# Kernel optimization log

Hardware: AMD Instinct MI355X
Metric: run time of the kernel (lower is better)

The kernel has to match this reference:

```python
import jax, jax.numpy as jnp
import numpy as np
import math

W = 64  # window_size == chunk_size == 64


def _windows(x, w):
    """x: [b, t, ...] -> [b, nb, 2w, ...]: for block j, concat(block j-1, block j).
    Block -1 is zero padding; its validity is handled by the attention mask."""
    b, t = x.shape[0], x.shape[1]
    nb = t // w
    pad = [(0, 0), (w, 0)] + [(0, 0)] * (x.ndim - 2)
    xp = jnp.pad(x, pad)                                   # [b, t+w, ...]
    xb = xp.reshape((b, nb + 1, w) + x.shape[2:])          # [b, nb+1, w, ...]
    return jnp.concatenate([xb[:, :-1], xb[:, 1:]], axis=2)  # [b, nb, 2w, ...]


def setup_inputs() -> dict:
    key = jax.random.key(0)
    k1, k2, k3 = jax.random.split(key, 3)
    b, t, h, d = 4, 4096, 16, 64
    return {
        "q": jax.random.normal(k1, (b, t, h, d), dtype=jnp.float32),
        "k": jax.random.normal(k2, (b, t, h, d), dtype=jnp.float32),
        "v": jax.random.normal(k3, (b, t, h, d), dtype=jnp.float32),
        "attn_mask": jnp.ones((b, t), dtype=jnp.int32),
    }


def reference(q, k, v, attn_mask):
    b, t, h, d = q.shape
    nb = t // W
    scale = 1.0 / math.sqrt(d)

    qb = q.reshape(b, nb, W, h, d)
    kw = _windows(k, W)                         # [b, nb, 2W, h, d]
    vw = _windows(v, W)                         # [b, nb, 2W, h, d]
    mw = _windows(attn_mask.astype(bool), W)    # [b, nb, 2W]

    # query local index i attends to key local index m iff 0 <= (i+W-m) < W
    i = jnp.arange(W)[:, None]
    m = jnp.arange(2 * W)[None, :]
    diff = i + W - m
    band = (diff >= 0) & (diff < W)             # [W, 2W]

    valid = band[None, None] & mw[:, :, None, :]          # [b, nb, W, 2W]

    scores = jnp.einsum('bnqhd,bnkhd->bnhqk', qb, kw) * scale  # [b,nb,h,W,2W]
    scores = jnp.where(valid[:, :, None], scores, jnp.float32(-1e9))
    attn = jax.nn.softmax(scores, axis=-1)
    attn = attn * valid[:, :, None].astype(attn.dtype)

    qm = attn_mask.astype(q.dtype).reshape(b, nb, W)      # query validity
    attn = attn * qm[:, :, None, :, None]

    out = jnp.einsum('bnhqk,bnkhd->bnqhd', attn, vw)      # [b,nb,W,h,d]
    out = out * qm[:, :, :, None, None]
    return out.reshape(b, t, h, d)
```

## Files before the change

kernel.cpp:

```cpp
#include <hip/hip_runtime.h>
#include <hip/hip_bf16.h>


#define TT 4096
#define HH 16
#define DD 64
#define WW 64
#define NBLK (TT / WW)

typedef __attribute__((ext_vector_type(8))) short bf16x8;
typedef __attribute__((ext_vector_type(4))) float f32x4;

static __device__ __forceinline__ ushort f2bf(float x) {
    return __builtin_bit_cast(unsigned short, __float2bfloat16(x));
}
static __device__ __forceinline__ uint pack2(float a, float b) {
    return (uint)f2bf(a) | ((uint)f2bf(b) << 16);
}

__global__ __launch_bounds__(256, 3)
void lca_fwd(const float* __restrict__ q, const float* __restrict__ k,
             const float* __restrict__ v, const int* __restrict__ am,
             float* __restrict__ out)
{
    const int jb = blockIdx.x;
    const int hi = blockIdx.y;
    const int bi = blockIdx.z;

    __shared__ union {
        struct { ushort Q[64][72]; ushort K[128][72]; } qk;
        ushort P[64][136];
    } u;
    __shared__ ushort sVt[64][136];
    __shared__ int    sKv[128];
    __shared__ int    sQv[64];

    const int tid = threadIdx.x;
    const size_t rowstride = (size_t)HH * DD;
    const size_t qbase = ((size_t)(bi * TT + jb * WW) * HH + hi) * DD;
    const long  kstart = (long)jb * WW - WW;

    if (tid < 128) {
        long tok = kstart + tid;
        sKv[tid] = (tok >= 0) && (am[(size_t)bi * TT + tok] != 0);
    } else if (tid < 192) {
        int r = tid - 128;
        sQv[r] = (am[(size_t)bi * TT + jb * WW + r] != 0);
    }

    float4 fq[4], fk[8], fv[8];
    #pragma unroll
    for (int p = 0; p < 4; ++p) {
        int idx = p * 256 + tid;
        int row = idx >> 4, c4 = (idx & 15) * 4;
        fq[p] = *(const float4*)(q + qbase + (size_t)row * rowstride + c4);
    }
    if (jb > 0) {
        #pragma unroll
        for (int p = 0; p < 8; ++p) {
            int idx = p * 256 + tid;
            int row = idx >> 4, c4 = (idx & 15) * 4;
            fk[p] = *(const float4*)(k + ((size_t)(bi * TT + kstart + row) * HH + hi) * DD + c4);
        }
        #pragma unroll
        for (int p = 0; p < 8; ++p) {
            int idx = p * 256 + tid;
            int row = idx >> 4, c4 = (idx & 15) * 4;
            fv[p] = *(const float4*)(v + ((size_t)(bi * TT + kstart + row) * HH + hi) * DD + c4);
        }
    } else {
        #pragma unroll
        for (int p = 0; p < 8; ++p) {
            float4 z = make_float4(0.f, 0.f, 0.f, 0.f);
            if (p >= 4) {
                int idx = p * 256 + tid;
                int row = idx >> 4, c4 = (idx & 15) * 4;
                z = *(const float4*)(k + ((size_t)(bi * TT + (row - 64)) * HH + hi) * DD + c4);
            }
            fk[p] = z;
        }
        #pragma unroll
        for (int p = 0; p < 8; ++p) {
            float4 z = make_float4(0.f, 0.f, 0.f, 0.f);
            if (p >= 4) {
                int idx = p * 256 + tid;
                int row = idx >> 4, c4 = (idx & 15) * 4;
                z = *(const float4*)(v + ((size_t)(bi * TT + (row - 64)) * HH + hi) * DD + c4);
            }
            fv[p] = z;
        }
    }

    #pragma unroll
    for (int p = 0; p < 4; ++p) {
        int idx = p * 256 + tid;
        int row = idx >> 4, c4 = (idx & 15) * 4;
        uint2 w; w.x = pack2(fq[p].x, fq[p].y); w.y = pack2(fq[p].z, fq[p].w);
        *(uint2*)(&u.qk.Q[row][c4]) = w;
    }
    #pragma unroll
    for (int p = 0; p < 8; ++p) {
        int idx = p * 256 + tid;
        int row = idx >> 4, c4 = (idx & 15) * 4;
        uint2 w; w.x = pack2(fk[p].x, fk[p].y); w.y = pack2(fk[p].z, fk[p].w);
        *(uint2*)(&u.qk.K[row][c4]) = w;
    }
    #pragma unroll
    for (int p = 0; p < 8; ++p) {
        int idx = p * 256 + tid;
        int row = idx >> 4, c4 = (idx & 15) * 4;
        sVt[c4 + 0][row] = f2bf(fv[p].x);
        sVt[c4 + 1][row] = f2bf(fv[p].y);
        sVt[c4 + 2][row] = f2bf(fv[p].z);
        sVt[c4 + 3][row] = f2bf(fv[p].w);
    }
    __syncthreads();

    const int wv = tid >> 6, lane = tid & 63;
    const int quad = lane >> 4, l15 = lane & 15;
    const int r0 = 16 * wv + quad * 4;

    bf16x8 aq0 = *(const bf16x8*)(&u.qk.Q[16 * wv + l15][quad * 8]);
    bf16x8 aq1 = *(const bf16x8*)(&u.qk.Q[16 * wv + l15][32 + quad * 8]);

    f32x4 acc[8];
    #pragma unroll
    for (int kt = 0; kt < 8; ++kt) {
        f32x4 a = {0.f, 0.f, 0.f, 0.f};
        bf16x8 b0 = *(const bf16x8*)(&u.qk.K[16 * kt + l15][quad * 8]);
        bf16x8 b1 = *(const bf16x8*)(&u.qk.K[16 * kt + l15][32 + quad * 8]);
        a = __builtin_amdgcn_mfma_f32_16x16x32_bf16(aq0, b0, a, 0, 0, 0);
        a = __builtin_amdgcn_mfma_f32_16x16x32_bf16(aq1, b1, a, 0, 0, 0);
        acc[kt] = a;
    }
    __syncthreads();

    const float NEG = -1.0e9f;
    float rmax[4] = {NEG, NEG, NEG, NEG};
    #pragma unroll
    for (int kt = 0; kt < 8; ++kt) {
        int c = 16 * kt + l15;
        int kvc = sKv[c];
        #pragma unroll
        for (int reg = 0; reg < 4; ++reg) {
            int r = r0 + reg;
            bool valid = (c > r) && (c <= r + WW) && kvc;
            float s = valid ? acc[kt][reg] : NEG;
            acc[kt][reg] = s;
            rmax[reg] = fmaxf(rmax[reg], s);
        }
    }
    #pragma unroll
    for (int reg = 0; reg < 4; ++reg) {
        #pragma unroll
        for (int m = 1; m <= 8; m <<= 1)
            rmax[reg] = fmaxf(rmax[reg], __shfl_xor(rmax[reg], m, 64));
    }

    const float CEXP = 0.125f * 1.44269504088896f;
    float rsum[4] = {0.f, 0.f, 0.f, 0.f};
    #pragma unroll
    for (int kt = 0; kt < 8; ++kt) {
        int c = 16 * kt + l15;
        #pragma unroll
        for (int reg = 0; reg < 4; ++reg) {
            float s = acc[kt][reg];
            float pex = (s > -1.0e8f) ? exp2f((s - rmax[reg]) * CEXP) : 0.f;
            rsum[reg] += pex;
            u.P[r0 + reg][c] = f2bf(pex);
        }
    }
    float rden[4];
    #pragma unroll
    for (int reg = 0; reg < 4; ++reg) {
        #pragma unroll
        for (int m = 1; m <= 8; m <<= 1)
            rsum[reg] += __shfl_xor(rsum[reg], m, 64);
        rden[reg] = (rsum[reg] > 0.f ? 1.f / rsum[reg] : 0.f)
                    * (float)sQv[r0 + reg];
    }

    bf16x8 ap[4];
    #pragma unroll
    for (int kc = 0; kc < 4; ++kc)
        ap[kc] = *(const bf16x8*)(&u.P[16 * wv + l15][kc * 32 + quad * 8]);

    #pragma unroll
    for (int nt = 0; nt < 4; ++nt) {
        f32x4 a = {0.f, 0.f, 0.f, 0.f};
        #pragma unroll
        for (int kc = 0; kc < 4; ++kc) {
            bf16x8 bv = *(const bf16x8*)(&sVt[16 * nt + l15][kc * 32 + quad * 8]);
            a = __builtin_amdgcn_mfma_f32_16x16x32_bf16(ap[kc], bv, a, 0, 0, 0);
        }
        #pragma unroll
        for (int reg = 0; reg < 4; ++reg)
            out[qbase + (size_t)(r0 + reg) * rowstride + 16 * nt + l15]
                = a[reg] * rden[reg];
    }
}

extern "C" void kernel_launch(void* const* d_in, const int* in_sizes, int n_in,
                              void* d_out, int out_size, void* d_ws, size_t ws_size,
                              hipStream_t stream) {
    const float* q  = (const float*)d_in[0];
    const float* k  = (const float*)d_in[1];
    const float* v  = (const float*)d_in[2];
    const int*   am = (const int*)d_in[3];
    float* out = (float*)d_out;

    const int b = in_sizes[3] / TT;
    dim3 grid(NBLK, HH, b);
    dim3 block(256);
    lca_fwd<<<grid, block, 0, stream>>>(q, k, v, am, out);
}
```

Before: 228.5 us.

## Process two consecutive chunks per block, reusing shared K/V via XOR ring indexing

Each workgroup now handles two adjacent 64-token chunks, so the grid is halved. After the first chunk finishes, only the newer K/V half is overwritten in shared memory. The shared chunk is reached through XOR-swapped row and column indexing, which removes one redundant global load of K and V per chunk. The second chunk's Q/K/V are prefetched into registers before the first chunk's compute to overlap load latency. In exchange, register pressure rises and there are fewer, longer workgroups.

```diff
diff --git a/kernel.cpp b/kernel.cpp
--- a/kernel.cpp
+++ b/kernel.cpp
@@ -23,7 +23,7 @@
              const float* __restrict__ v, const int* __restrict__ am,
              float* __restrict__ out)
 {
-    const int jb = blockIdx.x;
+    const int jb0 = 2 * blockIdx.x, jb1 = jb0 + 1;
     const int hi = blockIdx.y;
     const int bi = blockIdx.z;
 
@@ -37,36 +37,29 @@
 
     const int tid = threadIdx.x;
     const size_t rowstride = (size_t)HH * DD;
-    const size_t qbase = ((size_t)(bi * TT + jb * WW) * HH + hi) * DD;
-    const long  kstart = (long)jb * WW - WW;
-
-    if (tid < 128) {
-        long tok = kstart + tid;
-        sKv[tid] = (tok >= 0) && (am[(size_t)bi * TT + tok] != 0);
-    } else if (tid < 192) {
-        int r = tid - 128;
-        sQv[r] = (am[(size_t)bi * TT + jb * WW + r] != 0);
-    }
+    const size_t qbase0 = ((size_t)(bi * TT + jb0 * WW) * HH + hi) * DD;
+    const size_t qbase1 = qbase0 + (size_t)WW * rowstride;
+    const long  kstart0 = (long)jb0 * WW - WW;
 
     float4 fq[4], fk[8], fv[8];
     #pragma unroll
     for (int p = 0; p < 4; ++p) {
         int idx = p * 256 + tid;
         int row = idx >> 4, c4 = (idx & 15) * 4;
-        fq[p] = *(const float4*)(q + qbase + (size_t)row * rowstride + c4);
-    }
-    if (jb > 0) {
+        fq[p] = *(const float4*)(q + qbase0 + (size_t)row * rowstride + c4);
+    }
+    if (jb0 > 0) {
         #pragma unroll
         for (int p = 0; p < 8; ++p) {
             int idx = p * 256 + tid;
             int row = idx >> 4, c4 = (idx & 15) * 4;
-            fk[p] = *(const float4*)(k + ((size_t)(bi * TT + kstart + row) * HH + hi) * DD + c4);
+            fk[p] = *(const float4*)(k + ((size_t)(bi * TT + kstart0 + row) * HH + hi) * DD + c4);
         }
         #pragma unroll
         for (int p = 0; p < 8; ++p) {
             int idx = p * 256 + tid;
             int row = idx >> 4, c4 = (idx & 15) * 4;
-            fv[p] = *(const float4*)(v + ((size_t)(bi * TT + kstart + row) * HH + hi) * DD + c4);
+            fv[p] = *(const float4*)(v + ((size_t)(bi * TT + kstart0 + row) * HH + hi) * DD + c4);
         }
     } else {
         #pragma unroll
@@ -90,7 +83,13 @@
             fv[p] = z;
         }
     }
-
+    if (tid < 128) {
+        long tok = kstart0 + tid;
+        sKv[tid] = (tok >= 0) && (am[(size_t)bi * TT + tok] != 0);
+    } else if (tid < 192) {
+        int r = tid - 128;
+        sQv[r] = (am[(size_t)bi * TT + jb0 * WW + r] != 0);
+    }
     #pragma unroll
     for (int p = 0; p < 4; ++p) {
         int idx = p * 256 + tid;
@@ -114,90 +113,126 @@
         sVt[c4 + 2][row] = f2bf(fv[p].z);
         sVt[c4 + 3][row] = f2bf(fv[p].w);
     }
+
+    float4 gq[4], gk[4], gv[4];
+    #pragma unroll
+    for (int p = 0; p < 4; ++p) {
+        int idx = p * 256 + tid;
+        int row = idx >> 4, c4 = (idx & 15) * 4;
+        gq[p] = *(const float4*)(q + qbase1 + (size_t)row * rowstride + c4);
+        gk[p] = *(const float4*)(k + ((size_t)(bi * TT + jb1 * WW + row) * HH + hi) * DD + c4);
+        gv[p] = *(const float4*)(v + ((size_t)(bi * TT + jb1 * WW + row) * HH + hi) * DD + c4);
+    }
     __syncthreads();
 
     const int wv = tid >> 6, lane = tid & 63;
     const int quad = lane >> 4, l15 = lane & 15;
     const int r0 = 16 * wv + quad * 4;
-
-    bf16x8 aq0 = *(const bf16x8*)(&u.qk.Q[16 * wv + l15][quad * 8]);
-    bf16x8 aq1 = *(const bf16x8*)(&u.qk.Q[16 * wv + l15][32 + quad * 8]);
-
-    f32x4 acc[8];
-    #pragma unroll
-    for (int kt = 0; kt < 8; ++kt) {
-        f32x4 a = {0.f, 0.f, 0.f, 0.f};
-        bf16x8 b0 = *(const bf16x8*)(&u.qk.K[16 * kt + l15][quad * 8]);
-        bf16x8 b1 = *(const bf16x8*)(&u.qk.K[16 * kt + l15][32 + quad * 8]);
-        a = __builtin_amdgcn_mfma_f32_16x16x32_bf16(aq0, b0, a, 0, 0, 0);
-        a = __builtin_amdgcn_mfma_f32_16x16x32_bf16(aq1, b1, a, 0, 0, 0);
-        acc[kt] = a;
-    }
+    const float NEG = -1.0e9f;
+    const float CEXP = 0.125f * 1.44269504088896f;
+
+    auto compute_tile = [&](int koff, size_t qb) {
+        bf16x8 aq0 = *(const bf16x8*)(&u.qk.Q[16 * wv + l15][quad * 8]);
+        bf16x8 aq1 = *(const bf16x8*)(&u.qk.Q[16 * wv + l15][32 + quad * 8]);
+        f32x4 acc[8];
+        #pragma unroll
+        for (int kt = 0; kt < 8; ++kt) {
+            f32x4 a = {0.f, 0.f, 0.f, 0.f};
+            int pr = (16 * kt + l15) ^ koff;
+            bf16x8 b0 = *(const bf16x8*)(&u.qk.K[pr][quad * 8]);
+            bf16x8 b1 = *(const bf16x8*)(&u.qk.K[pr][32 + quad * 8]);
+            a = __builtin_amdgcn_mfma_f32_16x16x32_bf16(aq0, b0, a, 0, 0, 0);
+            a = __builtin_amdgcn_mfma_f32_16x16x32_bf16(aq1, b1, a, 0, 0, 0);
+            acc[kt] = a;
+        }
+        __syncthreads();
+
+        float rmax[4] = {NEG, NEG, NEG, NEG};
+        #pragma unroll
+        for (int kt = 0; kt < 8; ++kt) {
+            int c = 16 * kt + l15;
+            int kvc = sKv[c];
+            #pragma unroll
+            for (int reg = 0; reg < 4; ++reg) {
+                int r = r0 + reg;
+                bool valid = (c > r) && (c <= r + WW) && kvc;
+                float s = valid ? acc[kt][reg] : NEG;
+                acc[kt][reg] = s;
+                rmax[reg] = fmaxf(rmax[reg], s);
+            }
+        }
+        #pragma unroll
+        for (int reg = 0; reg < 4; ++reg) {
+            #pragma unroll
+            for (int m = 1; m <= 8; m <<= 1)
+                rmax[reg] = fmaxf(rmax[reg], __shfl_xor(rmax[reg], m, 64));
+        }
+        float rsum[4] = {0.f, 0.f, 0.f, 0.f};
+        #pragma unroll
+        for (int kt = 0; kt < 8; ++kt) {
+            int c = 16 * kt + l15;
+            #pragma unroll
+            for (int reg = 0; reg < 4; ++reg) {
+                float s = acc[kt][reg];
+                float pex = (s > -1.0e8f) ? exp2f((s - rmax[reg]) * CEXP) : 0.f;
+                rsum[reg] += pex;
+                u.P[r0 + reg][c] = f2bf(pex);
+            }
+        }
+        float rden[4];
+        #pragma unroll
+        for (int reg = 0; reg < 4; ++reg) {
+            #pragma unroll
+            for (int m = 1; m <= 8; m <<= 1)
+                rsum[reg] += __shfl_xor(rsum[reg], m, 64);
+            rden[reg] = (rsum[reg] > 0.f ? 1.f / rsum[reg] : 0.f)
+                        * (float)sQv[r0 + reg];
+        }
+        bf16x8 ap[4];
+        #pragma unroll
+        for (int kc = 0; kc < 4; ++kc)
+            ap[kc] = *(const bf16x8*)(&u.P[16 * wv + l15][kc * 32 + quad * 8]);
+        #pragma unroll
+        for (int nt = 0; nt < 4; ++nt) {
+            f32x4 a = {0.f, 0.f, 0.f, 0.f};
+            #pragma unroll
+            for (int kc = 0; kc < 4; ++kc) {
+                int pc = (kc * 32 + quad * 8) ^ koff;
+                bf16x8 bv = *(const bf16x8*)(&sVt[16 * nt + l15][pc]);
+                a = __builtin_amdgcn_mfma_f32_16x16x32_bf16(ap[kc], bv, a, 0, 0, 0);
+            }
+            #pragma unroll
+            for (int reg = 0; reg < 4; ++reg)
+                out[qb + (size_t)(r0 + reg) * rowstride + 16 * nt + l15]
+                    = a[reg] * rden[reg];
+        }
+    };
+
+    compute_tile(0, qbase0);
     __syncthreads();
 
-    const float NEG = -1.0e9f;
-    float rmax[4] = {NEG, NEG, NEG, NEG};
-    #pragma unroll
-    for (int kt = 0; kt < 8; ++kt) {
-        int c = 16 * kt + l15;
-        int kvc = sKv[c];
-        #pragma unroll
-        for (int reg = 0; reg < 4; ++reg) {
-            int r = r0 + reg;
-            bool valid = (c > r) && (c <= r + WW) && kvc;
-            float s = valid ? acc[kt][reg] : NEG;
-            acc[kt][reg] = s;
-            rmax[reg] = fmaxf(rmax[reg], s);
-        }
-    }
-    #pragma unroll
-    for (int reg = 0; reg < 4; ++reg) {
-        #pragma unroll
-        for (int m = 1; m <= 8; m <<= 1)
-            rmax[reg] = fmaxf(rmax[reg], __shfl_xor(rmax[reg], m, 64));
-    }
-
-    const float CEXP = 0.125f * 1.44269504088896f;
-    float rsum[4] = {0.f, 0.f, 0.f, 0.f};
-    #pragma unroll
-    for (int kt = 0; kt < 8; ++kt) {
-        int c = 16 * kt + l15;
-        #pragma unroll
-        for (int reg = 0; reg < 4; ++reg) {
-            float s = acc[kt][reg];
-            float pex = (s > -1.0e8f) ? exp2f((s - rmax[reg]) * CEXP) : 0.f;
-            rsum[reg] += pex;
-            u.P[r0 + reg][c] = f2bf(pex);
-        }
-    }
-    float rden[4];
-    #pragma unroll
-    for (int reg = 0; reg < 4; ++reg) {
-        #pragma unroll
-        for (int m = 1; m <= 8; m <<= 1)
-            rsum[reg] += __shfl_xor(rsum[reg], m, 64);
-        rden[reg] = (rsum[reg] > 0.f ? 1.f / rsum[reg] : 0.f)
-                    * (float)sQv[r0 + reg];
-    }
-
-    bf16x8 ap[4];
-    #pragma unroll
-    for (int kc = 0; kc < 4; ++kc)
-        ap[kc] = *(const bf16x8*)(&u.P[16 * wv + l15][kc * 32 + quad * 8]);
-
-    #pragma unroll
-    for (int nt = 0; nt < 4; ++nt) {
-        f32x4 a = {0.f, 0.f, 0.f, 0.f};
-        #pragma unroll
-        for (int kc = 0; kc < 4; ++kc) {
-            bf16x8 bv = *(const bf16x8*)(&sVt[16 * nt + l15][kc * 32 + quad * 8]);
-            a = __builtin_amdgcn_mfma_f32_16x16x32_bf16(ap[kc], bv, a, 0, 0, 0);
-        }
-        #pragma unroll
-        for (int reg = 0; reg < 4; ++reg)
-            out[qbase + (size_t)(r0 + reg) * rowstride + 16 * nt + l15]
-                = a[reg] * rden[reg];
-    }
+    if (tid < 128) {
+        sKv[tid] = (am[(size_t)bi * TT + jb0 * WW + tid] != 0);
+    } else if (tid < 192) {
+        int r = tid - 128;
+        sQv[r] = (am[(size_t)bi * TT + jb1 * WW + r] != 0);
+    }
+    #pragma unroll
+    for (int p = 0; p < 4; ++p) {
+        int idx = p * 256 + tid;
+        int row = idx >> 4, c4 = (idx & 15) * 4;
+        uint2 w; w.x = pack2(gq[p].x, gq[p].y); w.y = pack2(gq[p].z, gq[p].w);
+        *(uint2*)(&u.qk.Q[row][c4]) = w;
+        uint2 wk; wk.x = pack2(gk[p].x, gk[p].y); wk.y = pack2(gk[p].z, gk[p].w);
+        *(uint2*)(&u.qk.K[row][c4]) = wk;
+        sVt[c4 + 0][row] = f2bf(gv[p].x);
+        sVt[c4 + 1][row] = f2bf(gv[p].y);
+        sVt[c4 + 2][row] = f2bf(gv[p].z);
+        sVt[c4 + 3][row] = f2bf(gv[p].w);
+    }
+    __syncthreads();
+
+    compute_tile(64, qbase1);
 }
 
 extern "C" void kernel_launch(void* const* d_in, const int* in_sizes, int n_in,
@@ -210,7 +245,7 @@
     float* out = (float*)d_out;
 
     const int b = in_sizes[3] / TT;
-    dim3 grid(NBLK, HH, b);
+    dim3 grid(NBLK / 2, HH, b);
     dim3 block(256);
     lca_fwd<<<grid, block, 0, stream>>>(q, k, v, am, out);
 }
```

Measured after the change: 243.0 us. 6.4% more time.

## Load Q fragments directly into registers, drop Q shared tile, raise occupancy

Applied to the files above, without the earlier changes.

Q is now read from global memory straight into the MFMA A-operand layout and packed to bf16 in registers, so the Q shared-memory tile and its round trip are removed. With less LDS per block, the launch bound is raised to 4 blocks per SM. The second barrier moves after the softmax, so that math overlaps instead of waiting, and the P stores are deferred until after it. The per-lane Q global loads are less coalesced (32-byte pieces per row), and the extra registers held under the higher occupancy target could cause spills.

```diff
diff --git a/kernel.cpp b/kernel.cpp
--- a/kernel.cpp
+++ b/kernel.cpp
@@ -18,7 +18,7 @@
     return (uint)f2bf(a) | ((uint)f2bf(b) << 16);
 }
 
-__global__ __launch_bounds__(256, 3)
+__global__ __launch_bounds__(256, 4)
 void lca_fwd(const float* __restrict__ q, const float* __restrict__ k,
              const float* __restrict__ v, const int* __restrict__ am,
              float* __restrict__ out)
@@ -28,7 +28,7 @@
     const int bi = blockIdx.z;
 
     __shared__ union {
-        struct { ushort Q[64][72]; ushort K[128][72]; } qk;
+        ushort K[128][72];
         ushort P[64][136];
     } u;
     __shared__ ushort sVt[64][136];
@@ -36,25 +36,15 @@
     __shared__ int    sQv[64];
 
     const int tid = threadIdx.x;
+    const int wv = tid >> 6, lane = tid & 63;
+    const int quad = lane >> 4, l15 = lane & 15;
+    const int r0 = 16 * wv + quad * 4;
+
     const size_t rowstride = (size_t)HH * DD;
     const size_t qbase = ((size_t)(bi * TT + jb * WW) * HH + hi) * DD;
     const long  kstart = (long)jb * WW - WW;
 
-    if (tid < 128) {
-        long tok = kstart + tid;
-        sKv[tid] = (tok >= 0) && (am[(size_t)bi * TT + tok] != 0);
-    } else if (tid < 192) {
-        int r = tid - 128;
-        sQv[r] = (am[(size_t)bi * TT + jb * WW + r] != 0);
-    }
-
-    float4 fq[4], fk[8], fv[8];
-    #pragma unroll
-    for (int p = 0; p < 4; ++p) {
-        int idx = p * 256 + tid;
-        int row = idx >> 4, c4 = (idx & 15) * 4;
-        fq[p] = *(const float4*)(q + qbase + (size_t)row * rowstride + c4);
-    }
+    float4 fk[8], fv[8];
     if (jb > 0) {
         #pragma unroll
         for (int p = 0; p < 8; ++p) {
@@ -90,20 +80,30 @@
             fv[p] = z;
         }
     }
-
-    #pragma unroll
-    for (int p = 0; p < 4; ++p) {
-        int idx = p * 256 + tid;
-        int row = idx >> 4, c4 = (idx & 15) * 4;
-        uint2 w; w.x = pack2(fq[p].x, fq[p].y); w.y = pack2(fq[p].z, fq[p].w);
-        *(uint2*)(&u.qk.Q[row][c4]) = w;
-    }
+    const float* qrow = q + qbase + (size_t)(16 * wv + l15) * rowstride + quad * 8;
+    float4 q0 = *(const float4*)(qrow);
+    float4 q1 = *(const float4*)(qrow + 4);
+    float4 q2 = *(const float4*)(qrow + 32);
+    float4 q3 = *(const float4*)(qrow + 36);
+
+#if __has_builtin(__builtin_amdgcn_sched_barrier)
+    __builtin_amdgcn_sched_barrier(0);
+#endif
+
+    if (tid < 128) {
+        long tok = kstart + tid;
+        sKv[tid] = (tok >= 0) && (am[(size_t)bi * TT + tok] != 0);
+    } else if (tid < 192) {
+        int r = tid - 128;
+        sQv[r] = (am[(size_t)bi * TT + jb * WW + r] != 0);
+    }
+
     #pragma unroll
     for (int p = 0; p < 8; ++p) {
         int idx = p * 256 + tid;
         int row = idx >> 4, c4 = (idx & 15) * 4;
         uint2 w; w.x = pack2(fk[p].x, fk[p].y); w.y = pack2(fk[p].z, fk[p].w);
-        *(uint2*)(&u.qk.K[row][c4]) = w;
+        *(uint2*)(&u.K[row][c4]) = w;
     }
     #pragma unroll
     for (int p = 0; p < 8; ++p) {
@@ -114,26 +114,26 @@
         sVt[c4 + 2][row] = f2bf(fv[p].z);
         sVt[c4 + 3][row] = f2bf(fv[p].w);
     }
+
+    union BF8 { bf16x8 v; uint u4[4]; };
+    BF8 A0, A1;
+    A0.u4[0] = pack2(q0.x, q0.y); A0.u4[1] = pack2(q0.z, q0.w);
+    A0.u4[2] = pack2(q1.x, q1.y); A0.u4[3] = pack2(q1.z, q1.w);
+    A1.u4[0] = pack2(q2.x, q2.y); A1.u4[1] = pack2(q2.z, q2.w);
+    A1.u4[2] = pack2(q3.x, q3.y); A1.u4[3] = pack2(q3.z, q3.w);
+
     __syncthreads();
 
-    const int wv = tid >> 6, lane = tid & 63;
-    const int quad = lane >> 4, l15 = lane & 15;
-    const int r0 = 16 * wv + quad * 4;
-
-    bf16x8 aq0 = *(const bf16x8*)(&u.qk.Q[16 * wv + l15][quad * 8]);
-    bf16x8 aq1 = *(const bf16x8*)(&u.qk.Q[16 * wv + l15][32 + quad * 8]);
-
     f32x4 acc[8];
     #pragma unroll
     for (int kt = 0; kt < 8; ++kt) {
         f32x4 a = {0.f, 0.f, 0.f, 0.f};
-        bf16x8 b0 = *(const bf16x8*)(&u.qk.K[16 * kt + l15][quad * 8]);
-        bf16x8 b1 = *(const bf16x8*)(&u.qk.K[16 * kt + l15][32 + quad * 8]);
-        a = __builtin_amdgcn_mfma_f32_16x16x32_bf16(aq0, b0, a, 0, 0, 0);
-        a = __builtin_amdgcn_mfma_f32_16x16x32_bf16(aq1, b1, a, 0, 0, 0);
+        bf16x8 b0 = *(const bf16x8*)(&u.K[16 * kt + l15][quad * 8]);
+        bf16x8 b1 = *(const bf16x8*)(&u.K[16 * kt + l15][32 + quad * 8]);
+        a = __builtin_amdgcn_mfma_f32_16x16x32_bf16(A0.v, b0, a, 0, 0, 0);
+        a = __builtin_amdgcn_mfma_f32_16x16x32_bf16(A1.v, b1, a, 0, 0, 0);
         acc[kt] = a;
     }
-    __syncthreads();
 
     const float NEG = -1.0e9f;
     float rmax[4] = {NEG, NEG, NEG, NEG};
@@ -156,18 +156,16 @@
         for (int m = 1; m <= 8; m <<= 1)
             rmax[reg] = fmaxf(rmax[reg], __shfl_xor(rmax[reg], m, 64));
     }
-
     const float CEXP = 0.125f * 1.44269504088896f;
     float rsum[4] = {0.f, 0.f, 0.f, 0.f};
     #pragma unroll
     for (int kt = 0; kt < 8; ++kt) {
-        int c = 16 * kt + l15;
         #pragma unroll
         for (int reg = 0; reg < 4; ++reg) {
             float s = acc[kt][reg];
             float pex = (s > -1.0e8f) ? exp2f((s - rmax[reg]) * CEXP) : 0.f;
             rsum[reg] += pex;
-            u.P[r0 + reg][c] = f2bf(pex);
+            acc[kt][reg] = pex;
         }
     }
     float rden[4];
@@ -178,6 +176,16 @@
             rsum[reg] += __shfl_xor(rsum[reg], m, 64);
         rden[reg] = (rsum[reg] > 0.f ? 1.f / rsum[reg] : 0.f)
                     * (float)sQv[r0 + reg];
+    }
+
+    __syncthreads();
+
+    #pragma unroll
+    for (int kt = 0; kt < 8; ++kt) {
+        int c = 16 * kt + l15;
+        #pragma unroll
+        for (int reg = 0; reg < 4; ++reg)
+            u.P[r0 + reg][c] = f2bf(acc[kt][reg]);
     }
 
     bf16x8 ap[4];
```

After: 229.0 us. About the same (+0.2%).
